# Kernel optimization log

Hardware: AMD Instinct MI355X
Metric: run time of the kernel (lower is better)

Reference implementation:

```python
import jax, jax.numpy as jnp
import numpy as np

BATCH = 8
NUM_GENES = 20000
NUM_GENESETS = 4096
FEAT = 64


def setup_inputs() -> dict:
    # Deterministic ragged geneset structure in CSR form (equivalent to the
    # module's genesets_indices list-of-lists).
    rng = np.random.default_rng(0)
    counts = rng.integers(10, 90, size=NUM_GENESETS)          # genes per geneset
    total = int(counts.sum())                                 # ~202k memberships
    flat_indices = rng.integers(0, NUM_GENES, size=total)     # concatenated geneset members
    segment_ids = np.repeat(np.arange(NUM_GENESETS), counts)  # geneset id per member (sorted)

    key = jax.random.key(0)
    gene_output = jax.random.normal(key, (BATCH, NUM_GENES, FEAT), dtype=jnp.float32)
    return {
        "gene_output": gene_output,
        "flat_indices": jnp.asarray(flat_indices, jnp.int32),
        "segment_ids": jnp.asarray(segment_ids, jnp.int32),
        "counts": jnp.asarray(counts, jnp.int32),
    }


def reference(gene_output, flat_indices, segment_ids, counts):
    # gene_output: [B, G, D]; fused gather over all geneset members, then a
    # single ragged segment mean (== per-geneset torch.mean in the loop).
    num_segments = counts.shape[0]
    gathered = gene_output[:, flat_indices, :]  # [B, total_members, D]
    sums = jax.vmap(
        lambda g: jax.ops.segment_sum(g, segment_ids, num_segments=num_segments)
    )(gathered)  # [B, num_genesets, D]
    return sums / counts.astype(gene_output.dtype)[None, :, None]
```

## Files before the change

kernel.cpp:

```cpp
#include <hip/hip_runtime.h>

#define BATCH 8
#define NUM_GENES 20000
#define FEAT 64

__global__ __launch_bounds__(256)
void find_starts_kernel(const int* __restrict__ segment_ids,
                        int* __restrict__ starts, int total)
{
    int i = blockIdx.x * 256 + threadIdx.x;
    if (i < total) {
        int s = segment_ids[i];
        if (i == 0 || segment_ids[i - 1] != s) starts[s] = i;
    }
}

__global__ __launch_bounds__(128, 8)
void genesets_pool_kernel(const float* __restrict__ gene,
                          const int*   __restrict__ flat_indices,
                          const int*   __restrict__ starts,
                          const int*   __restrict__ counts,
                          float*       __restrict__ out,
                          int num_segments)
{
    const int bid  = blockIdx.x;
    const int b    = bid & 7;
    const int wave = threadIdx.x >> 6;
    const int s    = (bid >> 3) * 2 + wave;
    const int lane = threadIdx.x & 63;
    const int sub  = lane >> 4;
    const int fq   = lane & 15;

    if (s >= num_segments) return;

    const int start = starts[s];
    const int cnt   = counts[s];

    int off_a = (lane      < cnt) ? flat_indices[start + lane]      * FEAT : 0;
    int off_b = (lane + 64 < cnt) ? flat_indices[start + lane + 64] * FEAT : 0;

    const float* gbase = gene + (size_t)b * NUM_GENES * FEAT + fq * 4;

    float4 acc = make_float4(0.f, 0.f, 0.f, 0.f);
    const int kn = (cnt + 3) >> 2;

    for (int c = 0; c < kn; c += 8) {
        float4 buf[8];
        #pragma unroll
        for (int p = 0; p < 8; ++p) {
            const int j = sub + 4 * (c + p);
            const int off = (j < 64) ? __shfl(off_a, j) : __shfl(off_b, j & 63);
            if (j < cnt) {
                buf[p] = *reinterpret_cast<const float4*>(gbase + off);
            } else {
                buf[p] = make_float4(0.f, 0.f, 0.f, 0.f);
            }
        }
        #pragma unroll
        for (int p = 0; p < 8; ++p) {
            acc.x += buf[p].x; acc.y += buf[p].y;
            acc.z += buf[p].z; acc.w += buf[p].w;
        }
    }

    acc.x += __shfl_xor(acc.x, 16); acc.y += __shfl_xor(acc.y, 16);
    acc.z += __shfl_xor(acc.z, 16); acc.w += __shfl_xor(acc.w, 16);
    acc.x += __shfl_xor(acc.x, 32); acc.y += __shfl_xor(acc.y, 32);
    acc.z += __shfl_xor(acc.z, 32); acc.w += __shfl_xor(acc.w, 32);

    if (sub == 0) {
        const float inv = 1.0f / (float)cnt;
        float4 r = make_float4(acc.x * inv, acc.y * inv, acc.z * inv, acc.w * inv);
        *reinterpret_cast<float4*>(out + ((size_t)b * num_segments + s) * FEAT + fq * 4) = r;
    }
}

extern "C" void kernel_launch(void* const* d_in, const int* in_sizes, int n_in,
                              void* d_out, int out_size, void* d_ws, size_t ws_size,
                              hipStream_t stream)
{
    const float* gene         = (const float*)d_in[0];
    const int*   flat_indices = (const int*)d_in[1];
    const int*   segment_ids  = (const int*)d_in[2];
    const int*   counts       = (const int*)d_in[3];
    float*       out          = (float*)d_out;

    const int total        = in_sizes[1];
    const int num_segments = in_sizes[3];

    int* starts = (int*)d_ws;

    find_starts_kernel<<<(total + 255) / 256, 256, 0, stream>>>(segment_ids, starts, total);

    const int seg_pairs = (num_segments + 1) / 2;
    const int nblocks   = seg_pairs * BATCH;
    genesets_pool_kernel<<<nblocks, 128, 0, stream>>>(gene, flat_indices, starts,
                                                      counts, out, num_segments);
}
```

Measured before the change: 32.93 us.

## Gather from a per-call bf16 copy of gene features to halve gather bytes

Adds a pre-pass that converts the fp32 gene tensor to bf16 in workspace, fused with the segment start detection. The pooling kernel then gathers 16-byte bf16 rows (8 features per lane) and accumulates in fp32. This is meant to halve the bytes moved by the random gather. In exchange it adds a full read and write pass over the input tensor each call and loses input precision. A fallback to the fp32 path runs when the workspace is too small.

```diff
diff --git a/kernel.cpp b/kernel.cpp
--- a/kernel.cpp
+++ b/kernel.cpp
@@ -3,6 +3,111 @@
 #define BATCH 8
 #define NUM_GENES 20000
 #define FEAT 64
+
+__device__ __forceinline__ unsigned bf_round(float f) {
+    unsigned u = __float_as_uint(f);
+    return (u + 0x7FFFu + ((u >> 16) & 1u)) >> 16;
+}
+
+__global__ __launch_bounds__(256)
+void convert_and_starts_kernel(const float* __restrict__ gene,
+                               const int*   __restrict__ segment_ids,
+                               unsigned short* __restrict__ bf,
+                               int* __restrict__ starts,
+                               int total, int nconv8)
+{
+    const int tid = blockIdx.x * 256 + threadIdx.x;
+    const int nth = gridDim.x * 256;
+
+    const float4* g4 = reinterpret_cast<const float4*>(gene);
+    uint4*        o4 = reinterpret_cast<uint4*>(bf);
+    for (int i = tid; i < nconv8; i += nth) {
+        const float4 a = g4[2 * i];
+        const float4 c = g4[2 * i + 1];
+        uint4 o;
+        o.x = bf_round(a.x) | (bf_round(a.y) << 16);
+        o.y = bf_round(a.z) | (bf_round(a.w) << 16);
+        o.z = bf_round(c.x) | (bf_round(c.y) << 16);
+        o.w = bf_round(c.z) | (bf_round(c.w) << 16);
+        o4[i] = o;
+    }
+    for (int i = tid; i < total; i += nth) {
+        int s = segment_ids[i];
+        if (i == 0 || segment_ids[i - 1] != s) starts[s] = i;
+    }
+}
+
+__global__ __launch_bounds__(128, 8)
+void genesets_pool_bf16_kernel(const unsigned short* __restrict__ bf,
+                               const int* __restrict__ flat_indices,
+                               const int* __restrict__ starts,
+                               const int* __restrict__ counts,
+                               float* __restrict__ out,
+                               int num_segments)
+{
+    const int bid  = blockIdx.x;
+    const int b    = bid & 7;
+    const int wave = threadIdx.x >> 6;
+    const int s    = (bid >> 3) * 2 + wave;
+    const int lane = threadIdx.x & 63;
+    const int sub  = lane >> 3;
+    const int fq   = lane & 7;
+
+    if (s >= num_segments) return;
+
+    const int start = starts[s];
+    const int cnt   = counts[s];
+
+    int off_a = (lane      < cnt) ? flat_indices[start + lane]      * FEAT : 0;
+    int off_b = (lane + 64 < cnt) ? flat_indices[start + lane + 64] * FEAT : 0;
+
+    const unsigned short* gbase = bf + (size_t)b * NUM_GENES * FEAT + fq * 8;
+
+    float a0 = 0.f, a1 = 0.f, a2 = 0.f, a3 = 0.f;
+    float a4 = 0.f, a5 = 0.f, a6 = 0.f, a7 = 0.f;
+
+    const int kn8 = (cnt + 7) >> 3;
+
+    for (int c = 0; c < kn8; c += 8) {
+        uint4 buf[8];
+        #pragma unroll
+        for (int p = 0; p < 8; ++p) {
+            const int j = sub + 8 * (c + p);
+            const int off = (j < 64) ? __shfl(off_a, j) : __shfl(off_b, j & 63);
+            if (j < cnt) {
+                buf[p] = *reinterpret_cast<const uint4*>(gbase + off);
+            } else {
+                buf[p] = make_uint4(0u, 0u, 0u, 0u);
+            }
+        }
+        #pragma unroll
+        for (int p = 0; p < 8; ++p) {
+            a0 += __uint_as_float(buf[p].x << 16);
+            a1 += __uint_as_float(buf[p].x & 0xFFFF0000u);
+            a2 += __uint_as_float(buf[p].y << 16);
+            a3 += __uint_as_float(buf[p].y & 0xFFFF0000u);
+            a4 += __uint_as_float(buf[p].z << 16);
+            a5 += __uint_as_float(buf[p].z & 0xFFFF0000u);
+            a6 += __uint_as_float(buf[p].w << 16);
+            a7 += __uint_as_float(buf[p].w & 0xFFFF0000u);
+        }
+    }
+
+    #pragma unroll
+    for (int m = 8; m <= 32; m <<= 1) {
+        a0 += __shfl_xor(a0, m); a1 += __shfl_xor(a1, m);
+        a2 += __shfl_xor(a2, m); a3 += __shfl_xor(a3, m);
+        a4 += __shfl_xor(a4, m); a5 += __shfl_xor(a5, m);
+        a6 += __shfl_xor(a6, m); a7 += __shfl_xor(a7, m);
+    }
+
+    if (sub == 0) {
+        const float inv = 1.0f / (float)cnt;
+        float* obase = out + ((size_t)b * num_segments + s) * FEAT + fq * 8;
+        *reinterpret_cast<float4*>(obase)     = make_float4(a0 * inv, a1 * inv, a2 * inv, a3 * inv);
+        *reinterpret_cast<float4*>(obase + 4) = make_float4(a4 * inv, a5 * inv, a6 * inv, a7 * inv);
+    }
+}
 
 __global__ __launch_bounds__(256)
 void find_starts_kernel(const int* __restrict__ segment_ids,
@@ -50,11 +155,8 @@
         for (int p = 0; p < 8; ++p) {
             const int j = sub + 4 * (c + p);
             const int off = (j < 64) ? __shfl(off_a, j) : __shfl(off_b, j & 63);
-            if (j < cnt) {
-                buf[p] = *reinterpret_cast<const float4*>(gbase + off);
-            } else {
-                buf[p] = make_float4(0.f, 0.f, 0.f, 0.f);
-            }
+            if (j < cnt) buf[p] = *reinterpret_cast<const float4*>(gbase + off);
+            else         buf[p] = make_float4(0.f, 0.f, 0.f, 0.f);
         }
         #pragma unroll
         for (int p = 0; p < 8; ++p) {
@@ -88,12 +190,25 @@
     const int total        = in_sizes[1];
     const int num_segments = in_sizes[3];
 
-    int* starts = (int*)d_ws;
-
-    find_starts_kernel<<<(total + 255) / 256, 256, 0, stream>>>(segment_ids, starts, total);
+    const size_t plane_bytes = (size_t)BATCH * NUM_GENES * FEAT * 2;
+    const size_t need        = plane_bytes + (size_t)num_segments * 4;
 
     const int seg_pairs = (num_segments + 1) / 2;
     const int nblocks   = seg_pairs * BATCH;
-    genesets_pool_kernel<<<nblocks, 128, 0, stream>>>(gene, flat_indices, starts,
-                                                      counts, out, num_segments);
-}
+
+    if (ws_size >= need) {
+        unsigned short* bf     = (unsigned short*)d_ws;
+        int*            starts = (int*)((char*)d_ws + plane_bytes);
+        const int nconv8 = BATCH * NUM_GENES * FEAT / 8;
+
+        convert_and_starts_kernel<<<2048, 256, 0, stream>>>(gene, segment_ids,
+                                                            bf, starts, total, nconv8);
+        genesets_pool_bf16_kernel<<<nblocks, 128, 0, stream>>>(bf, flat_indices, starts,
+                                                               counts, out, num_segments);
+    } else {
+        int* starts = (int*)d_ws;
+        find_starts_kernel<<<(total + 255) / 256, 256, 0, stream>>>(segment_ids, starts, total);
+        genesets_pool_kernel<<<nblocks, 128, 0, stream>>>(gene, flat_indices, starts,
+                                                          counts, out, num_segments);
+    }
+}
```

Result: slower. 47.05 us (+42.9%).
